# Optimization experiments

Hardware: AMD Instinct MI355X
Metric: run time of the kernel (lower is better)

Reference implementation:

```python
import jax, jax.numpy as jnp
import numpy as np

N = 4096
F_IN = 512
ALPHA = 0.2          # LeakyReLU negative slope
NEG_INF = -9e15      # mask fill used by pyGAT


def setup_inputs() -> dict:
    key = jax.random.key(0)
    ks = jax.random.split(key, 9)
    x = jax.random.normal(ks[0], (N, F_IN), dtype=jnp.float32)
    adj = (jax.random.uniform(ks[1], (N, N)) < 0.005).astype(jnp.float32)
    adj = jnp.maximum(adj, jnp.eye(N, dtype=jnp.float32))
    s = 0.05
    W1 = jax.random.normal(ks[2], (512, 8, 128), dtype=jnp.float32) * s
    a_src1 = jax.random.normal(ks[3], (8, 128), dtype=jnp.float32) * s
    a_dst1 = jax.random.normal(ks[4], (8, 128), dtype=jnp.float32) * s
    W2 = jax.random.normal(ks[5], (1024, 1, 16), dtype=jnp.float32) * s
    a_src2 = jax.random.normal(ks[6], (1, 16), dtype=jnp.float32) * s
    a_dst2 = jax.random.normal(ks[7], (1, 16), dtype=jnp.float32) * s
    return {"x": x, "adj": adj, "W1": W1, "a_src1": a_src1, "a_dst1": a_dst1,
            "W2": W2, "a_src2": a_src2, "a_dst2": a_dst2}


def gat_layer(x, mask, W, a_src, a_dst, concat, activation):
    # x: [N, Fin], W: [Fin, H, Fout]
    h = jnp.einsum('nf,fho->nho', x, W)                  # [N, H, Fout]
    f_src = jnp.einsum('nho,ho->hn', h, a_src)            # [H, N]
    f_dst = jnp.einsum('nho,ho->hn', h, a_dst)            # [H, N]
    e = f_src[:, :, None] + f_dst[:, None, :]             # [H, N, N]
    e = jax.nn.leaky_relu(e, ALPHA)
    e = jnp.where(mask[None, :, :], e, NEG_INF)
    attn = jax.nn.softmax(e, axis=-1)                     # masked softmax over neighbors j
    out = jnp.einsum('hij,jho->iho', attn, h)             # [N, H, Fout]
    if concat:
        out = out.reshape(out.shape[0], -1)               # [N, H*Fout]
    else:
        out = out.mean(axis=1)                            # [N, Fout]
    if activation:
        out = jax.nn.elu(out)
    return out


def reference(x, adj, W1, a_src1, a_dst1, W2, a_src2, a_dst2):
    mask = adj > 0
    h1 = gat_layer(x, mask, W1, a_src1, a_dst1, concat=True, activation=True)
    h2 = gat_layer(h1, mask, W2, a_src2, a_dst2, concat=False, activation=False)
    out = jax.nn.elu(h2)
    return jax.nn.log_softmax(out, axis=1)
```

## Files before the change

### kernel.cpp

```cpp
#include <hip/hip_runtime.h>
#include <hip/hip_bf16.h>
#include <hip/hip_fp16.h>

typedef __attribute__((ext_vector_type(8))) short short8;
typedef __attribute__((ext_vector_type(8))) _Float16 half8;
typedef __attribute__((ext_vector_type(4))) float f32x4;
typedef __attribute__((ext_vector_type(2))) float f32x2;

#define MAXNBR 128
#define ALPHA 0.2f

static __device__ __forceinline__ unsigned short f2h(float f) {
    return __half_as_ushort(__float2half(f));
}
static __device__ __forceinline__ float h2f(unsigned short u) {
    return __half2float(__ushort_as_half(u));
}

__global__ __launch_bounds__(256) void cvt(const float* __restrict__ x,
                                           unsigned short* __restrict__ xh,
                                           const float* __restrict__ W1,
                                           unsigned short* __restrict__ W1t) {
    __shared__ float tile[64][65];
    int b = blockIdx.x, t = threadIdx.x;
    if (b < 1024) {
        size_t base = (size_t)b * 2048 + t * 8;
        float4 v0 = *(const float4*)&x[base];
        float4 v1 = *(const float4*)&x[base + 4];
        short8 o;
        o[0] = f2h(v0.x); o[1] = f2h(v0.y); o[2] = f2h(v0.z); o[3] = f2h(v0.w);
        o[4] = f2h(v1.x); o[5] = f2h(v1.y); o[6] = f2h(v1.z); o[7] = f2h(v1.w);
        *(short8*)&xh[base] = o;
    } else {
        int tb = b - 1024;
        int tk = (tb >> 4) * 64, tc = (tb & 15) * 64;
        int g = t >> 6, cx = t & 63;
        #pragma unroll
        for (int r = 0; r < 16; ++r)
            tile[g * 16 + r][cx] = W1[(size_t)(tk + g * 16 + r) * 1024 + tc + cx];
        __syncthreads();
        #pragma unroll
        for (int r = 0; r < 16; ++r)
            W1t[(size_t)(tc + g * 16 + r) * 512 + tk + cx] = f2h(tile[cx][g * 16 + r]);
    }
}

__global__ __launch_bounds__(256) void gemm_scan(const unsigned short* __restrict__ A,
                                                 const unsigned short* __restrict__ Bt,
                                                 unsigned short* __restrict__ C,
                                                 unsigned char* __restrict__ h1q,
                                                 const float* __restrict__ adj,
                                                 int* __restrict__ nbr_idx,
                                                 int* __restrict__ nbr_cnt) {
    __shared__ unsigned short Asm[128 * 64];
    __shared__ unsigned short Bsm[64 * 64];
    __shared__ int wsum[4];
    int b = blockIdx.x;
    int tid = threadIdx.x;
    if (b < 512) {
        int lane = tid & 63;
        int w = tid >> 6;
        int wr = w >> 1, wc = w & 1;
        int rowBase = (b & 31) * 128, colBase = (b >> 5) * 64;
        int lr = lane >> 3;
        int lcs = ((lane & 7) ^ lr) * 8;
        f32x4 acc[4][2] = {};
        for (int k0 = 0; k0 < 512; k0 += 64) {
            #pragma unroll
            for (int i = 0; i < 4; ++i) {
                int rA = i * 32 + w * 8;
                __builtin_amdgcn_global_load_lds(
                    (const __attribute__((address_space(1))) void*)&A[(size_t)(rowBase + rA + lr) * 512 + k0 + lcs],
                    (__attribute__((address_space(3))) void*)&Asm[rA * 64],
                    16, 0, 0);
            }
            #pragma unroll
            for (int i = 0; i < 2; ++i) {
                int rB = i * 32 + w * 8;
                __builtin_amdgcn_global_load_lds(
                    (const __attribute__((address_space(1))) void*)&Bt[(size_t)(colBase + rB + lr) * 512 + k0 + lcs],
                    (__attribute__((address_space(3))) void*)&Bsm[rB * 64],
                    16, 0, 0);
            }
            __syncthreads();
            #pragma unroll
            for (int kk = 0; kk < 64; kk += 32) {
                half8 af[4], bfv[2];
                int kf = kk + (lane >> 4) * 8;
                #pragma unroll
                for (int m = 0; m < 4; ++m) {
                    int R = wr * 64 + m * 16 + (lane & 15);
                    af[m] = *(const half8*)&Asm[R * 64 + (kf ^ ((R & 7) << 3))];
                }
                #pragma unroll
                for (int n = 0; n < 2; ++n) {
                    int R = wc * 32 + n * 16 + (lane & 15);
                    bfv[n] = *(const half8*)&Bsm[R * 64 + (kf ^ ((R & 7) << 3))];
                }
                #pragma unroll
                for (int m = 0; m < 4; ++m)
                    #pragma unroll
                    for (int n = 0; n < 2; ++n)
                        acc[m][n] = __builtin_amdgcn_mfma_f32_16x16x32_f16(af[m], bfv[n], acc[m][n], 0, 0, 0);
            }
            __syncthreads();
        }
        int crow0 = rowBase + wr * 64, ccol0 = colBase + wc * 32;
        #pragma unroll
        for (int m = 0; m < 4; ++m)
            #pragma unroll
            for (int n = 0; n < 2; ++n) {
                int col = ccol0 + n * 16 + (lane & 15);
                int row0 = crow0 + m * 16 + (lane >> 4) * 4;
                #pragma unroll
                for (int r = 0; r < 4; ++r) {
                    float v = acc[m][n][r];
                    C[(size_t)(row0 + r) * 1024 + col] = f2h(v);
                    int w8 = __builtin_amdgcn_cvt_pk_fp8_f32(v, v, 0, false);
                    h1q[(size_t)(row0 + r) * 1024 + col] = (unsigned char)w8;
                }
            }
    } else {
        int row = b - 512;
        int t = tid;
        const float* arow = adj + (size_t)row * 4096;
        const float4* ap = (const float4*)(arow + t * 16);
        float4 v0 = ap[0], v1 = ap[1], v2 = ap[2], v3 = ap[3];
        unsigned mask = 0;
        #pragma unroll
        for (int q = 0; q < 4; ++q) {
            if (((const float*)&v0)[q] > 0.f) mask |= 1u << q;
            if (((const float*)&v1)[q] > 0.f) mask |= 1u << (4 + q);
            if (((const float*)&v2)[q] > 0.f) mask |= 1u << (8 + q);
            if (((const float*)&v3)[q] > 0.f) mask |= 1u << (12 + q);
        }
        int mycnt = __popc(mask);
        int lane = t & 63, w = t >> 6;
        int incl = mycnt;
        #pragma unroll
        for (int d = 1; d < 64; d <<= 1) {
            int nn = __shfl_up(incl, d);
            if (lane >= d) incl += nn;
        }
        if (lane == 63) wsum[w] = incl;
        __syncthreads();
        int base = (w > 0 ? wsum[0] : 0) + (w > 1 ? wsum[1] : 0) + (w > 2 ? wsum[2] : 0);
        int pos = base + incl - mycnt;
        #pragma unroll
        for (int q = 0; q < 16; ++q) {
            if (mask & (1u << q)) {
                if (pos < MAXNBR) nbr_idx[row * MAXNBR + pos] = t * 16 + q;
                ++pos;
            }
        }
        if (t == 255) {
            int tot = base + incl;
            nbr_cnt[row] = tot < MAXNBR ? tot : MAXNBR;
        }
    }
}

__global__ __launch_bounds__(256) void attn_coef2(const unsigned short* __restrict__ h1h,
                                                  const float* __restrict__ a_src,
                                                  const float* __restrict__ a_dst,
                                                  float* __restrict__ fsp,
                                                  float* __restrict__ fdp) {
    int t = threadIdx.x;
    int n = blockIdx.x * 4 + (t >> 6);
    int l = t & 63;
    int head = l >> 3;
    const unsigned short* src = h1h + (size_t)n * 1024 + l * 16;
    const float* as = a_src + head * 128 + (l & 7) * 16;
    const float* ad = a_dst + head * 128 + (l & 7) * 16;
    float ps = 0.f, pd = 0.f;
    #pragma unroll
    for (int q = 0; q < 4; ++q) {
        ushort4 v = *(const ushort4*)&src[q * 4];
        float4 a4 = *(const float4*)&as[q * 4];
        float4 d4 = *(const float4*)&ad[q * 4];
        float h0 = h2f(v.x), h1 = h2f(v.y), h2_ = h2f(v.z), h3 = h2f(v.w);
        ps += h0 * a4.x + h1 * a4.y + h2_ * a4.z + h3 * a4.w;
        pd += h0 * d4.x + h1 * d4.y + h2_ * d4.z + h3 * d4.w;
    }
    ps += __shfl_xor(ps, 1); ps += __shfl_xor(ps, 2); ps += __shfl_xor(ps, 4);
    pd += __shfl_xor(pd, 1); pd += __shfl_xor(pd, 2); pd += __shfl_xor(pd, 4);
    if ((l & 7) == 0) {
        fsp[n * 8 + head] = ps;
        fdp[n * 8 + head] = pd;
    }
}

__global__ __launch_bounds__(512) void aggregate8(const unsigned char* __restrict__ h1q,
                                                  const int* __restrict__ nbr_idx,
                                                  const int* __restrict__ nbr_cnt,
                                                  const float* __restrict__ fsp,
                                                  const float* __restrict__ fdp,
                                                  unsigned short* __restrict__ h1act) {
    __shared__ int nbrS[2][MAXNBR];
    __shared__ float e_s[2][8][MAXNBR];
    __shared__ _Float16 attwS[2][8][MAXNBR];
    __shared__ half8 partS[2][128];
    int t = threadIdx.x;
    int sub = t >> 8, tl = t & 255;
    int i = blockIdx.x * 2 + sub;
    int cnt = nbr_cnt[i];
    int* nbr = nbrS[sub];
    if (tl < MAXNBR) {
        int nb = (tl < cnt) ? nbr_idx[i * MAXNBR + tl] : 0;
        nbr[tl] = nb;
        if (tl < cnt) {
            float4 fs0 = *(const float4*)&fsp[i * 8];
            float4 fs1 = *(const float4*)&fsp[i * 8 + 4];
            float4 d0 = *(const float4*)&fdp[nb * 8];
            float4 d1 = *(const float4*)&fdp[nb * 8 + 4];
            float e0 = fs0.x + d0.x, e1 = fs0.y + d0.y, e2 = fs0.z + d0.z, e3 = fs0.w + d0.w;
            float e4 = fs1.x + d1.x, e5 = fs1.y + d1.y, e6 = fs1.z + d1.z, e7 = fs1.w + d1.w;
            e_s[sub][0][tl] = e0 > 0.f ? e0 : ALPHA * e0;
            e_s[sub][1][tl] = e1 > 0.f ? e1 : ALPHA * e1;
            e_s[sub][2][tl] = e2 > 0.f ? e2 : ALPHA * e2;
            e_s[sub][3][tl] = e3 > 0.f ? e3 : ALPHA * e3;
            e_s[sub][4][tl] = e4 > 0.f ? e4 : ALPHA * e4;
            e_s[sub][5][tl] = e5 > 0.f ? e5 : ALPHA * e5;
            e_s[sub][6][tl] = e6 > 0.f ? e6 : ALPHA * e6;
            e_s[sub][7][tl] = e7 > 0.f ? e7 : ALPHA * e7;
        } else {
            #pragma unroll
            for (int h = 0; h < 8; ++h) e_s[sub][h][tl] = -INFINITY;
        }
    }
    __syncthreads();
    {
        int h = tl >> 5, sl = tl & 31;
        float e[4];
        #pragma unroll
        for (int p = 0; p < 4; ++p) e[p] = e_s[sub][h][sl + p * 32];
        float m = fmaxf(fmaxf(e[0], e[1]), fmaxf(e[2], e[3]));
        #pragma unroll
        for (int off = 1; off < 32; off <<= 1) m = fmaxf(m, __shfl_xor(m, off));
        float wq[4], s = 0.f;
        #pragma unroll
        for (int p = 0; p < 4; ++p) {
            wq[p] = (e[p] == -INFINITY) ? 0.f : __expf(e[p] - m);
            s += wq[p];
        }
        #pragma unroll
        for (int off = 1; off < 32; off <<= 1) s += __shfl_xor(s, off);
        float inv = 1.f / s;
        #pragma unroll
        for (int p = 0; p < 4; ++p)
            attwS[sub][h][sl + p * 32] = (_Float16)(wq[p] * inv);
    }
    __syncthreads();
    int tf = tl & 127;
    int par = tl >> 7;
    int head = tf >> 4;
    const unsigned char* src = h1q + tf * 8;
    float acc[8] = {0.f, 0.f, 0.f, 0.f, 0.f, 0.f, 0.f, 0.f};
    int cntPad = (cnt + 1) & ~1;
    for (int j = par; j < cntPad; j += 2) {
        int nb = nbr[j];
        float wv = (float)attwS[sub][head][j];
        uint2 v = *(const uint2*)&src[(size_t)nb << 10];
        f32x2 p0 = __builtin_amdgcn_cvt_pk_f32_fp8((int)v.x, false);
        f32x2 p1 = __builtin_amdgcn_cvt_pk_f32_fp8((int)v.x, true);
        f32x2 p2 = __builtin_amdgcn_cvt_pk_f32_fp8((int)v.y, false);
        f32x2 p3 = __builtin_amdgcn_cvt_pk_f32_fp8((int)v.y, true);
        acc[0] += wv * p0[0]; acc[1] += wv * p0[1];
        acc[2] += wv * p1[0]; acc[3] += wv * p1[1];
        acc[4] += wv * p2[0]; acc[5] += wv * p2[1];
        acc[6] += wv * p3[0]; acc[7] += wv * p3[1];
    }
    if (par) {
        half8 st;
        #pragma unroll
        for (int q = 0; q < 8; ++q) st[q] = (_Float16)acc[q];
        partS[sub][tf] = st;
    }
    __syncthreads();
    if (!par) {
        half8 p0 = partS[sub][tf];
        short8 o;
        #pragma unroll
        for (int q = 0; q < 8; ++q) {
            float a = acc[q] + (float)p0[q];
            a = a > 0.f ? a : (__expf(a) - 1.f);
            o[q] = f2h(a);
        }
        *(short8*)&h1act[(size_t)i * 1024 + tf * 8] = o;
    }
}

__global__ __launch_bounds__(256) void layer2_mfma(const unsigned short* __restrict__ h1act,
                                                   const float* __restrict__ W2,
                                                   const float* __restrict__ a_src2,
                                                   const float* __restrict__ a_dst2,
                                                   float* __restrict__ h2,
                                                   float2* __restrict__ fsd2) {
    __shared__ unsigned short W2t[16 * 1032];
    __shared__ float pred[4][256];
    int t = threadIdx.x, lane = t & 63, w = t >> 6;
    int rowBase = blockIdx.x * 16;
    for (int idx = t; idx < 16384; idx += 256) {
        int k = idx >> 4, o = idx & 15;
        W2t[o * 1032 + k] = f2h(W2[idx]);
    }
    __syncthreads();
    f32x4 acc = {};
    int r0 = lane & 15, kg = (lane >> 4) * 8;
    #pragma unroll
    for (int kk = 0; kk < 256; kk += 32) {
        int k0 = w * 256 + kk;
        half8 af = *(const half8*)&h1act[(size_t)(rowBase + r0) * 1024 + k0 + kg];
        half8 bf = *(const half8*)&W2t[r0 * 1032 + k0 + kg];
        acc = __builtin_amdgcn_mfma_f32_16x16x32_f16(af, bf, acc, 0, 0, 0);
    }
    #pragma unroll
    for (int r = 0; r < 4; ++r)
        pred[w][((lane >> 4) * 4 + r) * 16 + (lane & 15)] = acc[r];
    __syncthreads();
    if (t < 256) {
        int row = t >> 4, col = t & 15;
        float s = pred[0][t] + pred[1][t] + pred[2][t] + pred[3][t];
        h2[(rowBase + row) * 16 + col] = s;
        float ps = s * a_src2[col];
        float pd = s * a_dst2[col];
        #pragma unroll
        for (int off = 1; off < 16; off <<= 1) {
            ps += __shfl_xor(ps, off);
            pd += __shfl_xor(pd, off);
        }
        if (col == 0) fsd2[rowBase + row] = make_float2(ps, pd);
    }
}

__global__ __launch_bounds__(256) void final_layer2(const float* __restrict__ h2,
                                                    const int* __restrict__ nbr_idx,
                                                    const int* __restrict__ nbr_cnt,
                                                    const float2* __restrict__ fsd2,
                                                    float* __restrict__ out) {
    __shared__ float attnS[4][MAXNBR];
    __shared__ int nbrS[4][MAXNBR];
    int t = threadIdx.x;
    int w = t >> 6, l = t & 63;
    int i = blockIdx.x * 4 + w;
    float* attn = attnS[w];
    int* nbr = nbrS[w];
    int cnt = nbr_cnt[i];
    float fsi = fsd2[i].x;
    #pragma unroll
    for (int j = l; j < MAXNBR; j += 64) {
        float e = -INFINITY;
        if (j < cnt) {
            int jj = nbr_idx[i * MAXNBR + j];
            nbr[j] = jj;
            float xv = fsi + fsd2[jj].y;
            e = xv > 0.f ? xv : ALPHA * xv;
        }
        attn[j] = e;
    }
    float m = fmaxf(attn[l], attn[l + 64]);
    #pragma unroll
    for (int off = 1; off < 64; off <<= 1) m = fmaxf(m, __shfl_xor(m, off));
    float s = 0.f;
    {
        float e0 = attn[l], e1 = attn[l + 64];
        if (e0 != -INFINITY) s += __expf(e0 - m);
        if (e1 != -INFINITY) s += __expf(e1 - m);
    }
    #pragma unroll
    for (int off = 1; off < 64; off <<= 1) s += __shfl_xor(s, off);
    #pragma unroll
    for (int j = l; j < MAXNBR; j += 64) {
        float e = attn[j];
        attn[j] = (e == -INFINITY) ? 0.f : __expf(e - m) / s;
    }
    int o = l & 15, p = l >> 4;
    float acc = 0.f;
    for (int j = p; j < cnt; j += 4)
        acc += attn[j] * h2[nbr[j] * 16 + o];
    acc += __shfl_xor(acc, 16);
    acc += __shfl_xor(acc, 32);
    if (l < 16) {
        float v = acc > 0.f ? acc : expm1f(acc);
        float mx = v;
        #pragma unroll
        for (int off = 1; off < 16; off <<= 1) mx = fmaxf(mx, __shfl_xor(mx, off));
        float se = __expf(v - mx);
        #pragma unroll
        for (int off = 1; off < 16; off <<= 1) se += __shfl_xor(se, off);
        out[i * 16 + l] = v - mx - logf(se);
    }
}

extern "C" void kernel_launch(void* const* d_in, const int* in_sizes, int n_in,
                              void* d_out, int out_size, void* d_ws, size_t ws_size,
                              hipStream_t stream) {
    const float* x      = (const float*)d_in[0];
    const float* adj    = (const float*)d_in[1];
    const float* W1     = (const float*)d_in[2];
    const float* a_src1 = (const float*)d_in[3];
    const float* a_dst1 = (const float*)d_in[4];
    const float* W2     = (const float*)d_in[5];
    const float* a_src2 = (const float*)d_in[6];
    const float* a_dst2 = (const float*)d_in[7];
    float* out = (float*)d_out;

    char* ws = (char*)d_ws;
    unsigned short* xh    = (unsigned short*)ws;
    unsigned short* w1t   = (unsigned short*)(ws + (4u << 20));
    unsigned short* h1h   = (unsigned short*)(ws + (6u << 20));
    float* fsp   = (float*)(ws + (14u << 20));
    float* fdp   = (float*)(ws + (14u << 20) + (128u << 10));
    float* h2    = (float*)(ws + (15u << 20));
    float2* fsd2 = (float2*)(ws + (15u << 20) + (256u << 10));
    int* nbr_idx = (int*)(ws + (16u << 20));
    int* nbr_cnt = (int*)(ws + (18u << 20));
    unsigned short* h1act = (unsigned short*)(ws + (26u << 20));
    unsigned char* h1q    = (unsigned char*)(ws + (34u << 20));

    cvt<<<1152, 256, 0, stream>>>(x, xh, W1, w1t);
    gemm_scan<<<4608, 256, 0, stream>>>(xh, w1t, h1h, h1q, adj, nbr_idx, nbr_cnt);
    attn_coef2<<<1024, 256, 0, stream>>>(h1h, a_src1, a_dst1, fsp, fdp);
    aggregate8<<<2048, 512, 0, stream>>>(h1q, nbr_idx, nbr_cnt, fsp, fdp, h1act);
    layer2_mfma<<<256, 256, 0, stream>>>(h1act, W2, a_src2, a_dst2, h2, fsd2);
    final_layer2<<<1024, 256, 0, stream>>>(h2, nbr_idx, nbr_cnt, fsd2, out);
}
```

Measured before the change: 64.35 us.

## Fold attention vectors into W1 to compute f_src/f_dst directly from x

Precomputes W1·a_src and W1·a_dst per head in the conversion kernel, then computes the layer-1 attention coefficients as a small x·(W a) MFMA inside the GEMM/scan launch instead of a separate pass over h1. This removes the fp16 h1 store, the attn_coef2 kernel launch, and its re-read of the 8MB h1 buffer. The trade-off is rounding W·a to fp16 before the product, which changes numerics slightly, plus extra blocks in the cvt and gemm launches.

```diff
diff --git a/kernel.cpp b/kernel.cpp
--- a/kernel.cpp
+++ b/kernel.cpp
@@ -20,7 +20,10 @@
 __global__ __launch_bounds__(256) void cvt(const float* __restrict__ x,
                                            unsigned short* __restrict__ xh,
                                            const float* __restrict__ W1,
-                                           unsigned short* __restrict__ W1t) {
+                                           unsigned short* __restrict__ W1t,
+                                           const float* __restrict__ a_src1,
+                                           const float* __restrict__ a_dst1,
+                                           unsigned short* __restrict__ w_sdT) {
     __shared__ float tile[64][65];
     int b = blockIdx.x, t = threadIdx.x;
     if (b < 1024) {
@@ -31,7 +34,7 @@
         o[0] = f2h(v0.x); o[1] = f2h(v0.y); o[2] = f2h(v0.z); o[3] = f2h(v0.w);
         o[4] = f2h(v1.x); o[5] = f2h(v1.y); o[6] = f2h(v1.z); o[7] = f2h(v1.w);
         *(short8*)&xh[base] = o;
-    } else {
+    } else if (b < 1152) {
         int tb = b - 1024;
         int tk = (tb >> 4) * 64, tc = (tb & 15) * 64;
         int g = t >> 6, cx = t & 63;
@@ -42,19 +45,39 @@
         #pragma unroll
         for (int r = 0; r < 16; ++r)
             W1t[(size_t)(tc + g * 16 + r) * 512 + tk + cx] = f2h(tile[cx][g * 16 + r]);
-    }
-}
+    } else {
+        int id = (b - 1152) * 256 + t;
+        int k = id >> 3, h = id & 7;
+        const float* wrow = W1 + (size_t)k * 1024 + h * 128;
+        const float* as = a_src1 + h * 128;
+        const float* ad = a_dst1 + h * 128;
+        float s = 0.f, d = 0.f;
+        #pragma unroll 8
+        for (int o = 0; o < 128; o += 4) {
+            float4 wv = *(const float4*)&wrow[o];
+            float4 a4 = *(const float4*)&as[o];
+            float4 d4 = *(const float4*)&ad[o];
+            s += wv.x * a4.x + wv.y * a4.y + wv.z * a4.z + wv.w * a4.w;
+            d += wv.x * d4.x + wv.y * d4.y + wv.z * d4.z + wv.w * d4.w;
+        }
+        w_sdT[h * 512 + k] = f2h(s);
+        w_sdT[(h + 8) * 512 + k] = f2h(d);
+    }
+}
+
+struct SmemG { unsigned short Asm[128 * 64]; unsigned short Bsm[64 * 64]; int wsum[4]; };
+struct SmemC { unsigned short BT[16 * 520]; float pred[4][256]; };
 
 __global__ __launch_bounds__(256) void gemm_scan(const unsigned short* __restrict__ A,
                                                  const unsigned short* __restrict__ Bt,
-                                                 unsigned short* __restrict__ C,
                                                  unsigned char* __restrict__ h1q,
                                                  const float* __restrict__ adj,
                                                  int* __restrict__ nbr_idx,
-                                                 int* __restrict__ nbr_cnt) {
-    __shared__ unsigned short Asm[128 * 64];
-    __shared__ unsigned short Bsm[64 * 64];
-    __shared__ int wsum[4];
+                                                 int* __restrict__ nbr_cnt,
+                                                 const unsigned short* __restrict__ w_sdT,
+                                                 float* __restrict__ fsp,
+                                                 float* __restrict__ fdp) {
+    __shared__ union { SmemG g; SmemC c; } sm;
     int b = blockIdx.x;
     int tid = threadIdx.x;
     if (b < 512) {
@@ -71,7 +94,7 @@
                 int rA = i * 32 + w * 8;
                 __builtin_amdgcn_global_load_lds(
                     (const __attribute__((address_space(1))) void*)&A[(size_t)(rowBase + rA + lr) * 512 + k0 + lcs],
-                    (__attribute__((address_space(3))) void*)&Asm[rA * 64],
+                    (__attribute__((address_space(3))) void*)&sm.g.Asm[rA * 64],
                     16, 0, 0);
             }
             #pragma unroll
@@ -79,7 +102,7 @@
                 int rB = i * 32 + w * 8;
                 __builtin_amdgcn_global_load_lds(
                     (const __attribute__((address_space(1))) void*)&Bt[(size_t)(colBase + rB + lr) * 512 + k0 + lcs],
-                    (__attribute__((address_space(3))) void*)&Bsm[rB * 64],
+                    (__attribute__((address_space(3))) void*)&sm.g.Bsm[rB * 64],
                     16, 0, 0);
             }
             __syncthreads();
@@ -90,12 +113,12 @@
                 #pragma unroll
                 for (int m = 0; m < 4; ++m) {
                     int R = wr * 64 + m * 16 + (lane & 15);
-                    af[m] = *(const half8*)&Asm[R * 64 + (kf ^ ((R & 7) << 3))];
+                    af[m] = *(const half8*)&sm.g.Asm[R * 64 + (kf ^ ((R & 7) << 3))];
                 }
                 #pragma unroll
                 for (int n = 0; n < 2; ++n) {
                     int R = wc * 32 + n * 16 + (lane & 15);
-                    bfv[n] = *(const half8*)&Bsm[R * 64 + (kf ^ ((R & 7) << 3))];
+                    bfv[n] = *(const half8*)&sm.g.Bsm[R * 64 + (kf ^ ((R & 7) << 3))];
                 }
                 #pragma unroll
                 for (int m = 0; m < 4; ++m)
@@ -115,12 +138,11 @@
                 #pragma unroll
                 for (int r = 0; r < 4; ++r) {
                     float v = acc[m][n][r];
-                    C[(size_t)(row0 + r) * 1024 + col] = f2h(v);
                     int w8 = __builtin_amdgcn_cvt_pk_fp8_f32(v, v, 0, false);
                     h1q[(size_t)(row0 + r) * 1024 + col] = (unsigned char)w8;
                 }
             }
-    } else {
+    } else if (b < 4608) {
         int row = b - 512;
         int t = tid;
         const float* arow = adj + (size_t)row * 4096;
@@ -142,9 +164,9 @@
             int nn = __shfl_up(incl, d);
             if (lane >= d) incl += nn;
         }
-        if (lane == 63) wsum[w] = incl;
+        if (lane == 63) sm.g.wsum[w] = incl;
         __syncthreads();
-        int base = (w > 0 ? wsum[0] : 0) + (w > 1 ? wsum[1] : 0) + (w > 2 ? wsum[2] : 0);
+        int base = (w > 0 ? sm.g.wsum[0] : 0) + (w > 1 ? sm.g.wsum[1] : 0) + (w > 2 ? sm.g.wsum[2] : 0);
         int pos = base + incl - mycnt;
         #pragma unroll
         for (int q = 0; q < 16; ++q) {
@@ -157,36 +179,34 @@
             int tot = base + incl;
             nbr_cnt[row] = tot < MAXNBR ? tot : MAXNBR;
         }
-    }
-}
-
-__global__ __launch_bounds__(256) void attn_coef2(const unsigned short* __restrict__ h1h,
-                                                  const float* __restrict__ a_src,
-                                                  const float* __restrict__ a_dst,
-                                                  float* __restrict__ fsp,
-                                                  float* __restrict__ fdp) {
-    int t = threadIdx.x;
-    int n = blockIdx.x * 4 + (t >> 6);
-    int l = t & 63;
-    int head = l >> 3;
-    const unsigned short* src = h1h + (size_t)n * 1024 + l * 16;
-    const float* as = a_src + head * 128 + (l & 7) * 16;
-    const float* ad = a_dst + head * 128 + (l & 7) * 16;
-    float ps = 0.f, pd = 0.f;
-    #pragma unroll
-    for (int q = 0; q < 4; ++q) {
-        ushort4 v = *(const ushort4*)&src[q * 4];
-        float4 a4 = *(const float4*)&as[q * 4];
-        float4 d4 = *(const float4*)&ad[q * 4];
-        float h0 = h2f(v.x), h1 = h2f(v.y), h2_ = h2f(v.z), h3 = h2f(v.w);
-        ps += h0 * a4.x + h1 * a4.y + h2_ * a4.z + h3 * a4.w;
-        pd += h0 * d4.x + h1 * d4.y + h2_ * d4.z + h3 * d4.w;
-    }
-    ps += __shfl_xor(ps, 1); ps += __shfl_xor(ps, 2); ps += __shfl_xor(ps, 4);
-    pd += __shfl_xor(pd, 1); pd += __shfl_xor(pd, 2); pd += __shfl_xor(pd, 4);
-    if ((l & 7) == 0) {
-        fsp[n * 8 + head] = ps;
-        fdp[n * 8 + head] = pd;
+    } else {
+        int t = tid, lane = t & 63, w = t >> 6;
+        int rowBase = (b - 4608) * 16;
+        for (int idx = t; idx < 8192; idx += 256) {
+            int c = idx >> 9, k = idx & 511;
+            sm.c.BT[c * 520 + k] = w_sdT[idx];
+        }
+        __syncthreads();
+        f32x4 acc = {};
+        int r0 = lane & 15, kg = (lane >> 4) * 8;
+        #pragma unroll
+        for (int kk = 0; kk < 128; kk += 32) {
+            int k0 = w * 128 + kk;
+            half8 af = *(const half8*)&A[(size_t)(rowBase + r0) * 512 + k0 + kg];
+            half8 bf = *(const half8*)&sm.c.BT[r0 * 520 + k0 + kg];
+            acc = __builtin_amdgcn_mfma_f32_16x16x32_f16(af, bf, acc, 0, 0, 0);
+        }
+        #pragma unroll
+        for (int r = 0; r < 4; ++r)
+            sm.c.pred[w][((lane >> 4) * 4 + r) * 16 + (lane & 15)] = acc[r];
+        __syncthreads();
+        {
+            int row = t >> 4, col = t & 15;
+            float s = sm.c.pred[0][t] + sm.c.pred[1][t] + sm.c.pred[2][t] + sm.c.pred[3][t];
+            int n = rowBase + row;
+            if (col < 8) fsp[n * 8 + col] = s;
+            else         fdp[n * 8 + col - 8] = s;
+        }
     }
 }
 
@@ -408,7 +428,7 @@
     char* ws = (char*)d_ws;
     unsigned short* xh    = (unsigned short*)ws;
     unsigned short* w1t   = (unsigned short*)(ws + (4u << 20));
-    unsigned short* h1h   = (unsigned short*)(ws + (6u << 20));
+    unsigned short* w_sdT = (unsigned short*)(ws + (5u << 20));
     float* fsp   = (float*)(ws + (14u << 20));
     float* fdp   = (float*)(ws + (14u << 20) + (128u << 10));
     float* h2    = (float*)(ws + (15u << 20));
@@ -418,9 +438,9 @@
     unsigned short* h1act = (unsigned short*)(ws + (26u << 20));
     unsigned char* h1q    = (unsigned char*)(ws + (34u << 20));
 
-    cvt<<<1152, 256, 0, stream>>>(x, xh, W1, w1t);
-    gemm_scan<<<4608, 256, 0, stream>>>(xh, w1t, h1h, h1q, adj, nbr_idx, nbr_cnt);
-    attn_coef2<<<1024, 256, 0, stream>>>(h1h, a_src1, a_dst1, fsp, fdp);
+    cvt<<<1168, 256, 0, stream>>>(x, xh, W1, w1t, a_src1, a_dst1, w_sdT);
+    gemm_scan<<<4864, 256, 0, stream>>>(xh, w1t, h1q, adj, nbr_idx, nbr_cnt,
+                                        w_sdT, fsp, fdp);
     aggregate8<<<2048, 512, 0, stream>>>(h1q, nbr_idx, nbr_cnt, fsp, fdp, h1act);
     layer2_mfma<<<256, 256, 0, stream>>>(h1act, W2, a_src2, a_dst2, h2, fsd2);
     final_layer2<<<1024, 256, 0, stream>>>(h2, nbr_idx, nbr_cnt, fsd2, out);
```

Result: slower. 71.79 us (+11.6%).
